# Kernel optimization log

Hardware: AMD Instinct MI355X
Metric: run time of the kernel (lower is better)

## Reference

```python
import jax, jax.numpy as jnp
import numpy as np

D = 43           # d_model for '80k'
H1 = 30          # dense1
H2 = 20          # dense2
FEAT = 8


def _lstm_dir(x, w_ih, w_hh, b_ih, b_hh, reverse):
    # x: [B, T, I]; w_ih: [4H, I]; w_hh: [4H, H]; PyTorch gate order i,f,g,o
    B = x.shape[0]
    H = w_hh.shape[1]
    xs = jnp.swapaxes(x, 0, 1)                 # [T, B, I]
    b = b_ih + b_hh
    xz = xs @ w_ih.T + b                        # precompute input GEMM: [T, B, 4H]

    def step(carry, zt):
        h, c = carry
        z = zt + h @ w_hh.T
        i, f, g, o = jnp.split(z, 4, axis=-1)
        i = jax.nn.sigmoid(i); f = jax.nn.sigmoid(f)
        g = jnp.tanh(g);       o = jax.nn.sigmoid(o)
        c = f * c + i * g
        h = o * jnp.tanh(c)
        return (h, c), h

    h0 = jnp.zeros((B, H), x.dtype)
    _, hs = jax.lax.scan(step, (h0, h0), xz, reverse=reverse)
    return jnp.swapaxes(hs, 0, 1)               # [B, T, H]


def _bilstm(x, wf, wb):
    fwd = _lstm_dir(x, *wf, reverse=False)
    bwd = _lstm_dir(x, *wb, reverse=True)
    return jnp.concatenate([fwd, bwd], axis=-1)  # [B, T, 2H]


def setup_inputs() -> dict:
    key = jax.random.key(0)
    ks = iter(jax.random.split(key, 32))
    s = 0.1
    def rn(shape):
        return (jax.random.normal(next(ks), shape, dtype=jnp.float32) * s)
    inp = {"x": jax.random.normal(next(ks), (256, 2048, FEAT), dtype=jnp.float32)}
    # input projection (LazyLinear -> Linear(FEAT, D))
    inp["w_proj"] = rn((D, FEAT)); inp["b_proj"] = rn((D,))
    # lstm1: input D, hidden D, bidirectional
    for tag, isz in (("1f", D), ("1b", D), ("2f", 2 * D), ("2b", 2 * D)):
        inp[f"w_ih{tag}"] = rn((4 * D, isz))
        inp[f"w_hh{tag}"] = rn((4 * D, D))
        inp[f"b_ih{tag}"] = rn((4 * D,))
        inp[f"b_hh{tag}"] = rn((4 * D,))
    inp["w_d1"] = rn((H1, 2 * D)); inp["b_d1"] = rn((H1,))
    inp["w_d2"] = rn((H2, H1));    inp["b_d2"] = rn((H2,))
    inp["w_out"] = rn((1, H2));    inp["b_out"] = rn((1,))
    return inp


def reference(x, w_proj, b_proj,
              w_ih1f, w_hh1f, b_ih1f, b_hh1f,
              w_ih1b, w_hh1b, b_ih1b, b_hh1b,
              w_ih2f, w_hh2f, b_ih2f, b_hh2f,
              w_ih2b, w_hh2b, b_ih2b, b_hh2b,
              w_d1, b_d1, w_d2, b_d2, w_out, b_out):
    h = x @ w_proj.T + b_proj                                   # [B,T,D]
    h = _bilstm(h, (w_ih1f, w_hh1f, b_ih1f, b_hh1f),
                   (w_ih1b, w_hh1b, b_ih1b, b_hh1b))            # [B,T,2D]
    h = _bilstm(h, (w_ih2f, w_hh2f, b_ih2f, b_hh2f),
                   (w_ih2b, w_hh2b, b_ih2b, b_hh2b))            # [B,T,2D]
    h = jax.nn.relu(h @ w_d1.T + b_d1)
    h = jax.nn.relu(h @ w_d2.T + b_d2)
    return h @ w_out.T + b_out                                  # [B,T,1]
```

## Files before the change

### kernel.cpp

```cpp
#include <hip/hip_runtime.h>
#include <hip/hip_bf16.h>
#include <math.h>

#define DD   43
#define RR   172
#define TT   2048
#define BB   256
#define FEAT 8
#define NH1  30
#define NH2  20

using bf16 = __hip_bfloat16;

__device__ __forceinline__ float ldv(const float* p)  { return *p; }
__device__ __forceinline__ float ldv(const bf16* p)   { return __bfloat162float(*p); }
__device__ __forceinline__ void  stv(float* p, float v) { *p = v; }
__device__ __forceinline__ void  stv(bf16* p,  float v) { *p = __float2bfloat16(v); }

__device__ __forceinline__ float sig_(float x) {
    return 1.0f / (1.0f + __expf(-x));
}
__device__ __forceinline__ float tanh_(float x) {
    float ax = fabsf(x);
    float e  = __expf(-2.0f * ax);
    float t  = (1.0f - e) / (1.0f + e);
    return x < 0.0f ? -t : t;
}

__global__ void prep_kernel(const float* __restrict__ wp, const float* __restrict__ bp,
                            const float* __restrict__ w_ih1f, const float* __restrict__ b_ih1f, const float* __restrict__ b_hh1f,
                            const float* __restrict__ w_ih1b, const float* __restrict__ b_ih1b, const float* __restrict__ b_hh1b,
                            const float* __restrict__ b_ih2f, const float* __restrict__ b_hh2f,
                            const float* __restrict__ b_ih2b, const float* __restrict__ b_hh2b,
                            float* __restrict__ w_eff1, float* __restrict__ b_eff1,
                            float* __restrict__ b_eff2) {
    int tid = blockIdx.x * blockDim.x + threadIdx.x;
    if (tid < 2 * RR) {
        int dir = tid / RR, r = tid % RR;
        const float* w_ih = dir ? w_ih1b : w_ih1f;
        const float* bi   = dir ? b_ih1b : b_ih1f;
        const float* bh   = dir ? b_hh1b : b_hh1f;
        const float* row  = w_ih + (long)r * DD;
        float acc[FEAT];
#pragma unroll
        for (int k = 0; k < FEAT; ++k) acc[k] = 0.0f;
        float bacc = bi[r] + bh[r];
        for (int d = 0; d < DD; ++d) {
            float w = row[d];
            bacc = fmaf(w, bp[d], bacc);
#pragma unroll
            for (int k = 0; k < FEAT; ++k) acc[k] = fmaf(w, wp[d * FEAT + k], acc[k]);
        }
#pragma unroll
        for (int k = 0; k < FEAT; ++k) w_eff1[(long)tid * FEAT + k] = acc[k];
        b_eff1[tid] = bacc;
    } else if (tid < 4 * RR) {
        int j = tid - 2 * RR;
        int dir = j / RR, r = j % RR;
        b_eff2[j] = dir ? (b_ih2b[r] + b_hh2b[r]) : (b_ih2f[r] + b_hh2f[r]);
    }
}

template <int KI, typename TIN, typename TOUT>
__global__ __launch_bounds__(192) void lstm_kernel(
        const TIN* __restrict__ in,
        const float* __restrict__ w_ih_f,
        const float* __restrict__ w_hh_f,
        const float* __restrict__ bias_f,
        const float* __restrict__ w_ih_b,
        const float* __restrict__ w_hh_b,
        const float* __restrict__ bias_b,
        TOUT* __restrict__ out)
{
    const int bid = blockIdx.x;
    const int dir = bid & 1;
    const int b   = bid >> 1;
    const int tid = threadIdx.x;

    const float* w_ih = dir ? w_ih_b : w_ih_f;
    const float* w_hh = dir ? w_hh_b : w_hh_f;
    const float* bias = dir ? bias_b : bias_f;

    __shared__ float xbuf[2][KI];
    __shared__ float hbuf[DD];
    __shared__ float zbuf[RR];

    float wi[KI];
    float wh[DD];
    float bsum = 0.0f, c = 0.0f;
    if (tid < RR) {
        const float* wr = w_ih + (long)tid * KI;
#pragma unroll
        for (int k = 0; k < KI; ++k) wi[k] = wr[k];
        const float* hr = w_hh + (long)tid * DD;
#pragma unroll
        for (int k = 0; k < DD; ++k) wh[k] = hr[k];
        bsum = bias[tid];
    }

    const long t0   = dir ? (TT - 1) : 0;
    const int  step = dir ? -1 : 1;

    if (tid < DD) hbuf[tid] = 0.0f;
    float xnext = 0.0f;
    if (tid < KI) xnext = ldv(&in[((long)b * TT + t0) * KI + tid]);

    TOUT* outp = out + (long)b * TT * (2 * DD) + dir * DD;

    __syncthreads();

    long tcur = t0;
    for (int s = 0; s < TT; ++s) {
        if (tid < KI) xbuf[s & 1][tid] = xnext;
        __syncthreads();

        if (tid < RR) {
            float z = bsum;
            const float* xb = xbuf[s & 1];
#pragma unroll
            for (int k = 0; k < KI; ++k) z = fmaf(wi[k], xb[k], z);
#pragma unroll
            for (int k = 0; k < DD; ++k) z = fmaf(wh[k], hbuf[k], z);
            zbuf[tid] = z;
        }
        long tnext = tcur + step;
        if (s + 1 < TT && tid < KI) xnext = ldv(&in[((long)b * TT + tnext) * KI + tid]);
        __syncthreads();

        if (tid < DD) {
            float zi = zbuf[tid];
            float zf = zbuf[tid + DD];
            float zg = zbuf[tid + 2 * DD];
            float zo = zbuf[tid + 3 * DD];
            float ig = sig_(zi), fg = sig_(zf), gg = tanh_(zg), og = sig_(zo);
            c = fmaf(fg, c, ig * gg);
            float h = og * tanh_(c);
            hbuf[tid] = h;
            stv(&outp[tcur * (2 * DD) + tid], h);
        }
        tcur = tnext;
    }
}

template <typename TIN>
__global__ void head_kernel(const TIN* __restrict__ h2,
                            const float* __restrict__ w1, const float* __restrict__ b1,
                            const float* __restrict__ w2, const float* __restrict__ b2,
                            const float* __restrict__ w3, const float* __restrict__ b3,
                            float* __restrict__ outp) {
    long bt = (long)blockIdx.x * blockDim.x + threadIdx.x;
    if (bt >= (long)BB * TT) return;
    float v[2 * DD];
    const TIN* src = h2 + bt * (2 * DD);
#pragma unroll
    for (int k = 0; k < 2 * DD; ++k) v[k] = ldv(&src[k]);

    float m1[NH1];
#pragma unroll
    for (int j = 0; j < NH1; ++j) {
        float a = b1[j];
        const float* w = w1 + j * (2 * DD);
#pragma unroll
        for (int k = 0; k < 2 * DD; ++k) a = fmaf(w[k], v[k], a);
        m1[j] = fmaxf(a, 0.0f);
    }
    float m2[NH2];
#pragma unroll
    for (int j = 0; j < NH2; ++j) {
        float a = b2[j];
        const float* w = w2 + j * NH1;
#pragma unroll
        for (int k = 0; k < NH1; ++k) a = fmaf(w[k], m1[k], a);
        m2[j] = fmaxf(a, 0.0f);
    }
    float a = b3[0];
#pragma unroll
    for (int k = 0; k < NH2; ++k) a = fmaf(w3[k], m2[k], a);
    outp[bt] = a;
}

extern "C" void kernel_launch(void* const* d_in, const int* in_sizes, int n_in,
                              void* d_out, int out_size, void* d_ws, size_t ws_size,
                              hipStream_t stream) {
    const float* x      = (const float*)d_in[0];
    const float* w_proj = (const float*)d_in[1];
    const float* b_proj = (const float*)d_in[2];
    const float* w_ih1f = (const float*)d_in[3];
    const float* w_hh1f = (const float*)d_in[4];
    const float* b_ih1f = (const float*)d_in[5];
    const float* b_hh1f = (const float*)d_in[6];
    const float* w_ih1b = (const float*)d_in[7];
    const float* w_hh1b = (const float*)d_in[8];
    const float* b_ih1b = (const float*)d_in[9];
    const float* b_hh1b = (const float*)d_in[10];
    const float* w_ih2f = (const float*)d_in[11];
    const float* w_hh2f = (const float*)d_in[12];
    const float* b_ih2f = (const float*)d_in[13];
    const float* b_hh2f = (const float*)d_in[14];
    const float* w_ih2b = (const float*)d_in[15];
    const float* w_hh2b = (const float*)d_in[16];
    const float* b_ih2b = (const float*)d_in[17];
    const float* b_hh2b = (const float*)d_in[18];
    const float* w_d1   = (const float*)d_in[19];
    const float* b_d1   = (const float*)d_in[20];
    const float* w_d2   = (const float*)d_in[21];
    const float* b_d2   = (const float*)d_in[22];
    const float* w_out  = (const float*)d_in[23];
    const float* b_out  = (const float*)d_in[24];
    (void)in_sizes; (void)n_in; (void)out_size;

    float* w_eff1 = (float*)d_ws;
    float* b_eff1 = w_eff1 + 2 * RR * FEAT;
    float* b_eff2 = b_eff1 + 2 * RR;
    char*  big    = (char*)d_ws + 16384;
    size_t avail  = ws_size > 16384 ? ws_size - 16384 : 0;

    const size_t n1 = (size_t)BB * TT * 2 * DD;
    const size_t f1 = n1 * sizeof(float);
    const size_t h1 = n1 * sizeof(bf16);

    int tier;
    if      (avail >= f1 + f1) tier = 0;
    else if (avail >= f1 + h1) tier = 1;
    else                       tier = 2;

    prep_kernel<<<(4 * RR + 191) / 192, 192, 0, stream>>>(
        w_proj, b_proj,
        w_ih1f, b_ih1f, b_hh1f, w_ih1b, b_ih1b, b_hh1b,
        b_ih2f, b_hh2f, b_ih2b, b_hh2b,
        w_eff1, b_eff1, b_eff2);

    const float* weff_f = w_eff1;
    const float* weff_b = w_eff1 + (size_t)RR * FEAT;
    const float* be1_f  = b_eff1;
    const float* be1_b  = b_eff1 + RR;
    const float* be2_f  = b_eff2;
    const float* be2_b  = b_eff2 + RR;
    const int head_blocks = (int)(((long)BB * TT + 255) / 256);

    if (tier == 0) {
        float* out1 = (float*)big;
        float* out2 = (float*)(big + f1);
        lstm_kernel<FEAT, float, float><<<2 * BB, 192, 0, stream>>>(
            x, weff_f, w_hh1f, be1_f, weff_b, w_hh1b, be1_b, out1);
        lstm_kernel<2 * DD, float, float><<<2 * BB, 192, 0, stream>>>(
            out1, w_ih2f, w_hh2f, be2_f, w_ih2b, w_hh2b, be2_b, out2);
        head_kernel<float><<<head_blocks, 256, 0, stream>>>(
            out2, w_d1, b_d1, w_d2, b_d2, w_out, b_out, (float*)d_out);
    } else if (tier == 1) {
        float* out1 = (float*)big;
        bf16*  out2 = (bf16*)(big + f1);
        lstm_kernel<FEAT, float, float><<<2 * BB, 192, 0, stream>>>(
            x, weff_f, w_hh1f, be1_f, weff_b, w_hh1b, be1_b, out1);
        lstm_kernel<2 * DD, float, bf16><<<2 * BB, 192, 0, stream>>>(
            out1, w_ih2f, w_hh2f, be2_f, w_ih2b, w_hh2b, be2_b, out2);
        head_kernel<bf16><<<head_blocks, 256, 0, stream>>>(
            out2, w_d1, b_d1, w_d2, b_d2, w_out, b_out, (float*)d_out);
    } else {
        bf16* out1 = (bf16*)big;
        bf16* out2 = (bf16*)(big + h1);
        lstm_kernel<FEAT, float, bf16><<<2 * BB, 192, 0, stream>>>(
            x, weff_f, w_hh1f, be1_f, weff_b, w_hh1b, be1_b, out1);
        lstm_kernel<2 * DD, bf16, bf16><<<2 * BB, 192, 0, stream>>>(
            out1, w_ih2f, w_hh2f, be2_f, w_ih2b, w_hh2b, be2_b, out2);
        head_kernel<bf16><<<head_blocks, 256, 0, stream>>>(
            out2, w_d1, b_d1, w_d2, b_d2, w_out, b_out, (float*)d_out);
    }
}
```

Measured before the change: 3.973 ms.

## Split LSTM gate dot products across thread pairs with vectorized shared loads

Each gate row's dot product over the concatenated [x, h] vector is now split between two threads, which combine partial sums with a lane shuffle. Blocks grow from 192 to 384 threads. Inputs and hidden state share one double-buffered, float4-aligned shared-memory vector, so reads are vectorized and accumulation uses four independent chains. Gate activations move into the row threads, which leaves only the cell update on the 43 state threads and shortens the serial critical path per timestep. In exchange it adds a shuffle, padding work and more threads per block, which may limit occupancy.

Result: faster. 3.262 ms (-17.9%).

```diff
diff --git a/kernel.cpp b/kernel.cpp
--- a/kernel.cpp
+++ b/kernel.cpp
@@ -62,7 +62,7 @@
 }
 
 template <int KI, typename TIN, typename TOUT>
-__global__ __launch_bounds__(192) void lstm_kernel(
+__global__ __launch_bounds__(384, 3) void lstm_kernel(
         const TIN* __restrict__ in,
         const float* __restrict__ w_ih_f,
         const float* __restrict__ w_hh_f,
@@ -72,6 +72,11 @@
         const float* __restrict__ bias_b,
         TOUT* __restrict__ out)
 {
+    constexpr int K    = KI + DD;
+    constexpr int K4   = (K + 3) / 4;
+    constexpr int H0   = (K4 + 1) / 2;
+    constexpr int KPAD = 8 * H0;
+
     const int bid = blockIdx.x;
     const int dir = bid & 1;
     const int b   = bid >> 1;
@@ -81,64 +86,86 @@
     const float* w_hh = dir ? w_hh_b : w_hh_f;
     const float* bias = dir ? bias_b : bias_f;
 
-    __shared__ float xbuf[2][KI];
-    __shared__ float hbuf[DD];
+    __shared__ __align__(16) float sbuf[2][KPAD];
     __shared__ float zbuf[RR];
 
-    float wi[KI];
-    float wh[DD];
+    const int r  = tid >> 1;
+    const int hf = tid & 1;
+    const int g0 = hf ? H0 : 0;
+    const int gN = hf ? (K4 - H0) : H0;
+
+    float w[4 * H0];
     float bsum = 0.0f, c = 0.0f;
-    if (tid < RR) {
-        const float* wr = w_ih + (long)tid * KI;
-#pragma unroll
-        for (int k = 0; k < KI; ++k) wi[k] = wr[k];
-        const float* hr = w_hh + (long)tid * DD;
-#pragma unroll
-        for (int k = 0; k < DD; ++k) wh[k] = hr[k];
-        bsum = bias[tid];
-    }
-
-    const long t0   = dir ? (TT - 1) : 0;
-    const int  step = dir ? -1 : 1;
-
-    if (tid < DD) hbuf[tid] = 0.0f;
+    if (tid < 2 * RR) {
+#pragma unroll
+        for (int g = 0; g < H0; ++g) {
+#pragma unroll
+            for (int j = 0; j < 4; ++j) {
+                int k = 4 * (g0 + g) + j;
+                float v = 0.0f;
+                if (g < gN && k < K)
+                    v = (k < KI) ? w_ih[(long)r * KI + k]
+                                 : w_hh[(long)r * DD + (k - KI)];
+                w[4 * g + j] = v;
+            }
+        }
+        if (hf == 0) bsum = bias[r];
+    }
+    for (int k = KI + tid; k < KPAD; k += 384) {
+        sbuf[0][k] = 0.0f;
+        sbuf[1][k] = 0.0f;
+    }
+
+    const long t0  = dir ? (TT - 1) : 0;
+    const int  stp = dir ? -1 : 1;
+
     float xnext = 0.0f;
-    if (tid < KI) xnext = ldv(&in[((long)b * TT + t0) * KI + tid]);
+    if (tid < KI) xnext = ldv(in + ((long)b * TT + t0) * KI + tid);
 
     TOUT* outp = out + (long)b * TT * (2 * DD) + dir * DD;
 
     __syncthreads();
 
-    long tcur = t0;
+    long t = t0;
     for (int s = 0; s < TT; ++s) {
-        if (tid < KI) xbuf[s & 1][tid] = xnext;
+        const int cur = s & 1, nxt = cur ^ 1;
+        if (tid < KI) sbuf[cur][tid] = xnext;
         __syncthreads();
 
-        if (tid < RR) {
-            float z = bsum;
-            const float* xb = xbuf[s & 1];
-#pragma unroll
-            for (int k = 0; k < KI; ++k) z = fmaf(wi[k], xb[k], z);
-#pragma unroll
-            for (int k = 0; k < DD; ++k) z = fmaf(wh[k], hbuf[k], z);
-            zbuf[tid] = z;
-        }
-        long tnext = tcur + step;
-        if (s + 1 < TT && tid < KI) xnext = ldv(&in[((long)b * TT + tnext) * KI + tid]);
+        const long tn = t + stp;
+        if (s + 1 < TT && tid < KI) xnext = ldv(in + ((long)b * TT + tn) * KI + tid);
+
+        if (tid < 2 * RR) {
+            const float4* sv = reinterpret_cast<const float4*>(&sbuf[cur][0]) + g0;
+            float a0 = bsum, a1 = 0.0f, a2 = 0.0f, a3 = 0.0f;
+#pragma unroll
+            for (int g = 0; g < H0; ++g) {
+                float4 xv = sv[g];
+                a0 = fmaf(w[4 * g + 0], xv.x, a0);
+                a1 = fmaf(w[4 * g + 1], xv.y, a1);
+                a2 = fmaf(w[4 * g + 2], xv.z, a2);
+                a3 = fmaf(w[4 * g + 3], xv.w, a3);
+            }
+            float z = (a0 + a1) + (a2 + a3);
+            z += __shfl_xor(z, 1);
+            if (hf == 0) {
+                float act = (r >= 2 * DD && r < 3 * DD) ? tanh_(z) : sig_(z);
+                zbuf[r] = act;
+            }
+        }
         __syncthreads();
 
         if (tid < DD) {
-            float zi = zbuf[tid];
-            float zf = zbuf[tid + DD];
-            float zg = zbuf[tid + 2 * DD];
-            float zo = zbuf[tid + 3 * DD];
-            float ig = sig_(zi), fg = sig_(zf), gg = tanh_(zg), og = sig_(zo);
+            float ig = zbuf[tid];
+            float fg = zbuf[tid + DD];
+            float gg = zbuf[tid + 2 * DD];
+            float og = zbuf[tid + 3 * DD];
             c = fmaf(fg, c, ig * gg);
             float h = og * tanh_(c);
-            hbuf[tid] = h;
-            stv(&outp[tcur * (2 * DD) + tid], h);
-        }
-        tcur = tnext;
+            sbuf[nxt][KI + tid] = h;
+            stv(&outp[t * (2 * DD) + tid], h);
+        }
+        t = tn;
     }
 }
 
@@ -241,27 +268,27 @@
     if (tier == 0) {
         float* out1 = (float*)big;
         float* out2 = (float*)(big + f1);
-        lstm_kernel<FEAT, float, float><<<2 * BB, 192, 0, stream>>>(
+        lstm_kernel<FEAT, float, float><<<2 * BB, 384, 0, stream>>>(
             x, weff_f, w_hh1f, be1_f, weff_b, w_hh1b, be1_b, out1);
-        lstm_kernel<2 * DD, float, float><<<2 * BB, 192, 0, stream>>>(
+        lstm_kernel<2 * DD, float, float><<<2 * BB, 384, 0, stream>>>(
             out1, w_ih2f, w_hh2f, be2_f, w_ih2b, w_hh2b, be2_b, out2);
         head_kernel<float><<<head_blocks, 256, 0, stream>>>(
             out2, w_d1, b_d1, w_d2, b_d2, w_out, b_out, (float*)d_out);
     } else if (tier == 1) {
         float* out1 = (float*)big;
         bf16*  out2 = (bf16*)(big + f1);
-        lstm_kernel<FEAT, float, float><<<2 * BB, 192, 0, stream>>>(
+        lstm_kernel<FEAT, float, float><<<2 * BB, 384, 0, stream>>>(
             x, weff_f, w_hh1f, be1_f, weff_b, w_hh1b, be1_b, out1);
-        lstm_kernel<2 * DD, float, bf16><<<2 * BB, 192, 0, stream>>>(
+        lstm_kernel<2 * DD, float, bf16><<<2 * BB, 384, 0, stream>>>(
             out1, w_ih2f, w_hh2f, be2_f, w_ih2b, w_hh2b, be2_b, out2);
         head_kernel<bf16><<<head_blocks, 256, 0, stream>>>(
             out2, w_d1, b_d1, w_d2, b_d2, w_out, b_out, (float*)d_out);
     } else {
         bf16* out1 = (bf16*)big;
         bf16* out2 = (bf16*)(big + h1);
-        lstm_kernel<FEAT, float, bf16><<<2 * BB, 192, 0, stream>>>(
+        lstm_kernel<FEAT, float, bf16><<<2 * BB, 384, 0, stream>>>(
             x, weff_f, w_hh1f, be1_f, weff_b, w_hh1b, be1_b, out1);
-        lstm_kernel<2 * DD, bf16, bf16><<<2 * BB, 192, 0, stream>>>(
+        lstm_kernel<2 * DD, bf16, bf16><<<2 * BB, 384, 0, stream>>>(
             out1, w_ih2f, w_hh2f, be2_f, w_ih2b, w_hh2b, be2_b, out2);
         head_kernel<bf16><<<head_blocks, 256, 0, stream>>>(
             out2, w_d1, b_d1, w_d2, b_d2, w_out, b_out, (float*)d_out);
```

## Batch LSTM recurrence over 16 sequences per block using bf16 MFMA

Applied to the files above, without the earlier changes.

Replaces the per-sequence scalar FMA LSTM kernel with a block that handles 16 batch rows at once. At each timestep the input and recurrent projections run as bf16 16x16x32 MFMA ops against concatenated, padded weight fragments held in registers. A prep kernel builds the padded bf16 weight layouts, and both intermediate activations are now stored as bf16, dropping the fp32 tier logic. The intent is to raise arithmetic throughput and cut the sequential per-step cost. The trade-offs are reduced precision (bf16 weights, inputs and hidden state) and far fewer blocks, 32 instead of 512, leaving most CUs idle.

Measured after the change: 5.277 ms. +32.8%, slower.

```diff
diff --git a/kernel.cpp b/kernel.cpp
--- a/kernel.cpp
+++ b/kernel.cpp
@@ -4,22 +4,28 @@
 
 #define DD   43
 #define RR   172
+#define NPAD 176
 #define TT   2048
 #define BB   256
 #define FEAT 8
+#define MB   16
 #define NH1  30
 #define NH2  20
 
 using bf16 = __hip_bfloat16;
+typedef __attribute__((ext_vector_type(8))) short bf16x8;
+typedef __attribute__((ext_vector_type(4))) float f32x4;
 
 __device__ __forceinline__ float ldv(const float* p)  { return *p; }
 __device__ __forceinline__ float ldv(const bf16* p)   { return __bfloat162float(*p); }
 __device__ __forceinline__ void  stv(float* p, float v) { *p = v; }
 __device__ __forceinline__ void  stv(bf16* p,  float v) { *p = __float2bfloat16(v); }
 
-__device__ __forceinline__ float sig_(float x) {
-    return 1.0f / (1.0f + __expf(-x));
-}
+__device__ __forceinline__ short f2b(float f) {
+    bf16 h = __float2bfloat16(f);
+    return *reinterpret_cast<short*>(&h);
+}
+__device__ __forceinline__ float sig_(float x) { return 1.0f / (1.0f + __expf(-x)); }
 __device__ __forceinline__ float tanh_(float x) {
     float ax = fabsf(x);
     float e  = __expf(-2.0f * ax);
@@ -27,118 +33,229 @@
     return x < 0.0f ? -t : t;
 }
 
-__global__ void prep_kernel(const float* __restrict__ wp, const float* __restrict__ bp,
-                            const float* __restrict__ w_ih1f, const float* __restrict__ b_ih1f, const float* __restrict__ b_hh1f,
-                            const float* __restrict__ w_ih1b, const float* __restrict__ b_ih1b, const float* __restrict__ b_hh1b,
-                            const float* __restrict__ b_ih2f, const float* __restrict__ b_hh2f,
-                            const float* __restrict__ b_ih2b, const float* __restrict__ b_hh2b,
-                            float* __restrict__ w_eff1, float* __restrict__ b_eff1,
-                            float* __restrict__ b_eff2) {
-    int tid = blockIdx.x * blockDim.x + threadIdx.x;
-    if (tid < 2 * RR) {
-        int dir = tid / RR, r = tid % RR;
-        const float* w_ih = dir ? w_ih1b : w_ih1f;
-        const float* bi   = dir ? b_ih1b : b_ih1f;
-        const float* bh   = dir ? b_hh1b : b_hh1f;
-        const float* row  = w_ih + (long)r * DD;
-        float acc[FEAT];
-#pragma unroll
-        for (int k = 0; k < FEAT; ++k) acc[k] = 0.0f;
-        float bacc = bi[r] + bh[r];
-        for (int d = 0; d < DD; ++d) {
-            float w = row[d];
-            bacc = fmaf(w, bp[d], bacc);
-#pragma unroll
-            for (int k = 0; k < FEAT; ++k) acc[k] = fmaf(w, wp[d * FEAT + k], acc[k]);
-        }
-#pragma unroll
-        for (int k = 0; k < FEAT; ++k) w_eff1[(long)tid * FEAT + k] = acc[k];
-        b_eff1[tid] = bacc;
-    } else if (tid < 4 * RR) {
-        int j = tid - 2 * RR;
-        int dir = j / RR, r = j % RR;
-        b_eff2[j] = dir ? (b_ih2b[r] + b_hh2b[r]) : (b_ih2f[r] + b_hh2f[r]);
-    }
-}
-
-template <int KI, typename TIN, typename TOUT>
-__global__ __launch_bounds__(192) void lstm_kernel(
-        const TIN* __restrict__ in,
-        const float* __restrict__ w_ih_f,
-        const float* __restrict__ w_hh_f,
-        const float* __restrict__ bias_f,
-        const float* __restrict__ w_ih_b,
-        const float* __restrict__ w_hh_b,
-        const float* __restrict__ bias_b,
-        TOUT* __restrict__ out)
+__global__ void prep_kernel(
+    const float* __restrict__ wp, const float* __restrict__ bp,
+    const float* __restrict__ w_ih1f, const float* __restrict__ w_hh1f,
+    const float* __restrict__ b_ih1f, const float* __restrict__ b_hh1f,
+    const float* __restrict__ w_ih1b, const float* __restrict__ w_hh1b,
+    const float* __restrict__ b_ih1b, const float* __restrict__ b_hh1b,
+    const float* __restrict__ w_ih2f, const float* __restrict__ w_hh2f,
+    const float* __restrict__ b_ih2f, const float* __restrict__ b_hh2f,
+    const float* __restrict__ w_ih2b, const float* __restrict__ w_hh2b,
+    const float* __restrict__ b_ih2b, const float* __restrict__ b_hh2b,
+    short* __restrict__ W1, short* __restrict__ W2,
+    float* __restrict__ bias1, float* __restrict__ bias2)
 {
-    const int bid = blockIdx.x;
-    const int dir = bid & 1;
-    const int b   = bid >> 1;
-    const int tid = threadIdx.x;
-
-    const float* w_ih = dir ? w_ih_b : w_ih_f;
-    const float* w_hh = dir ? w_hh_b : w_hh_f;
-    const float* bias = dir ? bias_b : bias_f;
-
-    __shared__ float xbuf[2][KI];
-    __shared__ float hbuf[DD];
-    __shared__ float zbuf[RR];
-
-    float wi[KI];
-    float wh[DD];
-    float bsum = 0.0f, c = 0.0f;
-    if (tid < RR) {
-        const float* wr = w_ih + (long)tid * KI;
-#pragma unroll
-        for (int k = 0; k < KI; ++k) wi[k] = wr[k];
-        const float* hr = w_hh + (long)tid * DD;
-#pragma unroll
-        for (int k = 0; k < DD; ++k) wh[k] = hr[k];
-        bsum = bias[tid];
-    }
-
-    const long t0   = dir ? (TT - 1) : 0;
-    const int  step = dir ? -1 : 1;
-
-    if (tid < DD) hbuf[tid] = 0.0f;
-    float xnext = 0.0f;
-    if (tid < KI) xnext = ldv(&in[((long)b * TT + t0) * KI + tid]);
-
-    TOUT* outp = out + (long)b * TT * (2 * DD) + dir * DD;
-
+    const int S1 = 2 * NPAD * 96, S2 = 2 * NPAD * 160, S3 = 2 * NPAD;
+    int idx = blockIdx.x * blockDim.x + threadIdx.x;
+    if (idx < S1) {
+        int dir = idx / (NPAD * 96), rem = idx % (NPAD * 96);
+        int n = rem / 96, k = rem % 96;
+        const float* wih = dir ? w_ih1b : w_ih1f;
+        const float* whh = dir ? w_hh1b : w_hh1f;
+        float v = 0.0f;
+        if (n < RR) {
+            if (k < FEAT) {
+                for (int d = 0; d < DD; ++d) v = fmaf(wih[n * DD + d], wp[d * FEAT + k], v);
+            } else if (k >= 32 && k < 32 + DD) {
+                v = whh[n * DD + (k - 32)];
+            }
+        }
+        W1[idx] = f2b(v);
+    } else if (idx < S1 + S2) {
+        int j = idx - S1;
+        int dir = j / (NPAD * 160), rem = j % (NPAD * 160);
+        int n = rem / 160, k = rem % 160;
+        const float* wih = dir ? w_ih2b : w_ih2f;
+        const float* whh = dir ? w_hh2b : w_hh2f;
+        float v = 0.0f;
+        if (n < RR) {
+            if (k < 2 * DD)                 v = wih[n * (2 * DD) + k];
+            else if (k >= 96 && k < 96 + DD) v = whh[n * DD + (k - 96)];
+        }
+        W2[j] = f2b(v);
+    } else if (idx < S1 + S2 + S3) {
+        int j = idx - S1 - S2;
+        int dir = j / NPAD, n = j % NPAD;
+        float v = 0.0f;
+        if (n < RR) {
+            const float* wih = dir ? w_ih1b : w_ih1f;
+            const float* bi  = dir ? b_ih1b : b_ih1f;
+            const float* bh  = dir ? b_hh1b : b_hh1f;
+            v = bi[n] + bh[n];
+            for (int d = 0; d < DD; ++d) v = fmaf(wih[n * DD + d], bp[d], v);
+        }
+        bias1[j] = v;
+    } else if (idx < S1 + S2 + 2 * S3) {
+        int j = idx - S1 - S2 - S3;
+        int dir = j / NPAD, n = j % NPAD;
+        float v = 0.0f;
+        if (n < RR) {
+            const float* bi = dir ? b_ih2b : b_ih2f;
+            const float* bh = dir ? b_hh2b : b_hh2f;
+            v = bi[n] + bh[n];
+        }
+        bias2[j] = v;
+    }
+}
+
+template <int KSX, bool XRAW>
+__global__ __launch_bounds__(512, 2) void lstm_mfma(
+    const void*  __restrict__ in_,
+    const short* __restrict__ Wb,
+    const float* __restrict__ bias,
+    bf16* __restrict__ out)
+{
+    constexpr int KS   = KSX + 2;
+    constexpr int KPAD = KS * 32;
+
+    const int dir   = blockIdx.x & 1;
+    const int btile = blockIdx.x >> 1;
+    const int tid   = threadIdx.x;
+    const int lane  = tid & 63;
+    const int wv    = tid >> 6;
+    const int ln15  = lane & 15;
+    const int lg    = lane >> 4;
+
+    __shared__ __align__(16) short hbuf[MB][72];
+    __shared__ float zact[MB][177];
+
+    const int nt = (wv < 3) ? 2 : 1;
+
+    bf16x8 wfrag[2][KS];
+    float  bv[2];
+    bool   isg[2];
+    {
+        const short* Wd = Wb + (size_t)dir * NPAD * KPAD;
+#pragma unroll
+        for (int ti = 0; ti < 2; ++ti) {
+            int tile = ti ? (8 + wv) : wv;
+            int n = tile * 16 + ln15;
+            isg[ti] = (n >= 2 * DD && n < 3 * DD);
+            if (ti < nt) {
+#pragma unroll
+                for (int ks = 0; ks < KS; ++ks)
+                    wfrag[ti][ks] = *reinterpret_cast<const bf16x8*>(
+                        Wd + (size_t)n * KPAD + ks * 32 + lg * 8);
+                bv[ti] = bias[dir * NPAD + n];
+            } else {
+#pragma unroll
+                for (int ks = 0; ks < KS; ++ks) wfrag[ti][ks] = bf16x8(0);
+                bv[ti] = 0.0f;
+            }
+        }
+    }
+
+    const int p0 = tid;
+    const int b0 = p0 / DD, d0 = p0 % DD;
+    const int p1 = tid + 512;
+    const bool has1 = (p1 < MB * DD);
+    const int b1 = has1 ? p1 / DD : 0, d1 = has1 ? p1 % DD : 0;
+    float c0 = 0.0f, c1 = 0.0f;
+
+    for (int i = tid; i < MB * 72; i += 512) ((short*)hbuf)[i] = 0;
+
+    const long t00   = dir ? (TT - 1) : 0;
+    const int  stp   = dir ? -1 : 1;
+    const long bbase = (long)(btile * MB + ln15);
+
+    union U { unsigned u[4]; bf16x8 v; };
+    U xc[KSX], xn[KSX];
+
+    auto load_x = [&](long t, U (&xf)[KSX]) {
+        if constexpr (XRAW) {
+            if (lg == 0) {
+                const float* xp = (const float*)in_ + (bbase * TT + t) * FEAT;
+                float4 v0 = *reinterpret_cast<const float4*>(xp);
+                float4 v1 = *reinterpret_cast<const float4*>(xp + 4);
+                xf[0].u[0] = ((unsigned)(unsigned short)f2b(v0.y) << 16) | (unsigned short)f2b(v0.x);
+                xf[0].u[1] = ((unsigned)(unsigned short)f2b(v0.w) << 16) | (unsigned short)f2b(v0.z);
+                xf[0].u[2] = ((unsigned)(unsigned short)f2b(v1.y) << 16) | (unsigned short)f2b(v1.x);
+                xf[0].u[3] = ((unsigned)(unsigned short)f2b(v1.w) << 16) | (unsigned short)f2b(v1.z);
+            } else {
+#pragma unroll
+                for (int j = 0; j < 4; ++j) xf[0].u[j] = 0u;
+            }
+        } else {
+            const short* xp = (const short*)in_ + (bbase * TT + t) * (2 * DD);
+#pragma unroll
+            for (int ks = 0; ks < KSX; ++ks) {
+                int k0 = ks * 32 + lg * 8;
+#pragma unroll
+                for (int j = 0; j < 4; ++j) {
+                    int k = k0 + 2 * j;
+                    xf[ks].u[j] = (k < 2 * DD) ? *reinterpret_cast<const unsigned*>(xp + k) : 0u;
+                }
+            }
+        }
+    };
+
+    load_x(t00, xc);
     __syncthreads();
 
-    long tcur = t0;
+    long t = t00;
     for (int s = 0; s < TT; ++s) {
-        if (tid < KI) xbuf[s & 1][tid] = xnext;
+        bf16x8 ah0 = *reinterpret_cast<const bf16x8*>(&hbuf[ln15][lg * 8]);
+        bf16x8 ah1 = *reinterpret_cast<const bf16x8*>(&hbuf[ln15][32 + lg * 8]);
+        if (s + 1 < TT) load_x(t + stp, xn);
+
+        f32x4 acc0 = {bv[0], bv[0], bv[0], bv[0]};
+#pragma unroll
+        for (int ks = 0; ks < KSX; ++ks)
+            acc0 = __builtin_amdgcn_mfma_f32_16x16x32_bf16(xc[ks].v, wfrag[0][ks], acc0, 0, 0, 0);
+        acc0 = __builtin_amdgcn_mfma_f32_16x16x32_bf16(ah0, wfrag[0][KSX],     acc0, 0, 0, 0);
+        acc0 = __builtin_amdgcn_mfma_f32_16x16x32_bf16(ah1, wfrag[0][KSX + 1], acc0, 0, 0, 0);
+
+        f32x4 acc1 = {bv[1], bv[1], bv[1], bv[1]};
+        if (nt == 2) {
+#pragma unroll
+            for (int ks = 0; ks < KSX; ++ks)
+                acc1 = __builtin_amdgcn_mfma_f32_16x16x32_bf16(xc[ks].v, wfrag[1][ks], acc1, 0, 0, 0);
+            acc1 = __builtin_amdgcn_mfma_f32_16x16x32_bf16(ah0, wfrag[1][KSX],     acc1, 0, 0, 0);
+            acc1 = __builtin_amdgcn_mfma_f32_16x16x32_bf16(ah1, wfrag[1][KSX + 1], acc1, 0, 0, 0);
+        }
+
+        {
+            int n0 = wv * 16 + ln15;
+#pragma unroll
+            for (int r = 0; r < 4; ++r) {
+                float v = acc0[r];
+                zact[lg * 4 + r][n0] = isg[0] ? tanh_(v) : sig_(v);
+            }
+            if (nt == 2) {
+                int n1 = (8 + wv) * 16 + ln15;
+#pragma unroll
+                for (int r = 0; r < 4; ++r) {
+                    float v = acc1[r];
+                    zact[lg * 4 + r][n1] = isg[1] ? tanh_(v) : sig_(v);
+                }
+            }
+        }
         __syncthreads();
 
-        if (tid < RR) {
-            float z = bsum;
-            const float* xb = xbuf[s & 1];
-#pragma unroll
-            for (int k = 0; k < KI; ++k) z = fmaf(wi[k], xb[k], z);
-#pragma unroll
-            for (int k = 0; k < DD; ++k) z = fmaf(wh[k], hbuf[k], z);
-            zbuf[tid] = z;
-        }
-        long tnext = tcur + step;
-        if (s + 1 < TT && tid < KI) xnext = ldv(&in[((long)b * TT + tnext) * KI + tid]);
+        {
+            float ig = zact[b0][d0], fg = zact[b0][d0 + DD];
+            float gg = zact[b0][d0 + 2 * DD], og = zact[b0][d0 + 3 * DD];
+            c0 = fmaf(fg, c0, ig * gg);
+            float h = og * tanh_(c0);
+            hbuf[b0][d0] = f2b(h);
+            out[((long)(btile * MB + b0) * TT + t) * (2 * DD) + dir * DD + d0] = __float2bfloat16(h);
+            if (has1) {
+                float ig1 = zact[b1][d1], fg1 = zact[b1][d1 + DD];
+                float gg1 = zact[b1][d1 + 2 * DD], og1 = zact[b1][d1 + 3 * DD];
+                c1 = fmaf(fg1, c1, ig1 * gg1);
+                float h1 = og1 * tanh_(c1);
+                hbuf[b1][d1] = f2b(h1);
+                out[((long)(btile * MB + b1) * TT + t) * (2 * DD) + dir * DD + d1] = __float2bfloat16(h1);
+            }
+        }
         __syncthreads();
 
-        if (tid < DD) {
-            float zi = zbuf[tid];
-            float zf = zbuf[tid + DD];
-            float zg = zbuf[tid + 2 * DD];
-            float zo = zbuf[tid + 3 * DD];
-            float ig = sig_(zi), fg = sig_(zf), gg = tanh_(zg), og = sig_(zo);
-            c = fmaf(fg, c, ig * gg);
-            float h = og * tanh_(c);
-            hbuf[tid] = h;
-            stv(&outp[tcur * (2 * DD) + tid], h);
-        }
-        tcur = tnext;
+#pragma unroll
+        for (int ks = 0; ks < KSX; ++ks)
+#pragma unroll
+            for (int j = 0; j < 4; ++j) xc[ks].u[j] = xn[ks].u[j];
+        t += stp;
     }
 }
 
@@ -207,63 +324,28 @@
     const float* b_d2   = (const float*)d_in[22];
     const float* w_out  = (const float*)d_in[23];
     const float* b_out  = (const float*)d_in[24];
-    (void)in_sizes; (void)n_in; (void)out_size;
-
-    float* w_eff1 = (float*)d_ws;
-    float* b_eff1 = w_eff1 + 2 * RR * FEAT;
-    float* b_eff2 = b_eff1 + 2 * RR;
-    char*  big    = (char*)d_ws + 16384;
-    size_t avail  = ws_size > 16384 ? ws_size - 16384 : 0;
-
-    const size_t n1 = (size_t)BB * TT * 2 * DD;
-    const size_t f1 = n1 * sizeof(float);
-    const size_t h1 = n1 * sizeof(bf16);
-
-    int tier;
-    if      (avail >= f1 + f1) tier = 0;
-    else if (avail >= f1 + h1) tier = 1;
-    else                       tier = 2;
-
-    prep_kernel<<<(4 * RR + 191) / 192, 192, 0, stream>>>(
-        w_proj, b_proj,
-        w_ih1f, b_ih1f, b_hh1f, w_ih1b, b_ih1b, b_hh1b,
-        b_ih2f, b_hh2f, b_ih2b, b_hh2b,
-        w_eff1, b_eff1, b_eff2);
-
-    const float* weff_f = w_eff1;
-    const float* weff_b = w_eff1 + (size_t)RR * FEAT;
-    const float* be1_f  = b_eff1;
-    const float* be1_b  = b_eff1 + RR;
-    const float* be2_f  = b_eff2;
-    const float* be2_b  = b_eff2 + RR;
-    const int head_blocks = (int)(((long)BB * TT + 255) / 256);
-
-    if (tier == 0) {
-        float* out1 = (float*)big;
-        float* out2 = (float*)(big + f1);
-        lstm_kernel<FEAT, float, float><<<2 * BB, 192, 0, stream>>>(
-            x, weff_f, w_hh1f, be1_f, weff_b, w_hh1b, be1_b, out1);
-        lstm_kernel<2 * DD, float, float><<<2 * BB, 192, 0, stream>>>(
-            out1, w_ih2f, w_hh2f, be2_f, w_ih2b, w_hh2b, be2_b, out2);
-        head_kernel<float><<<head_blocks, 256, 0, stream>>>(
-            out2, w_d1, b_d1, w_d2, b_d2, w_out, b_out, (float*)d_out);
-    } else if (tier == 1) {
-        float* out1 = (float*)big;
-        bf16*  out2 = (bf16*)(big + f1);
-        lstm_kernel<FEAT, float, float><<<2 * BB, 192, 0, stream>>>(
-            x, weff_f, w_hh1f, be1_f, weff_b, w_hh1b, be1_b, out1);
-        lstm_kernel<2 * DD, float, bf16><<<2 * BB, 192, 0, stream>>>(
-            out1, w_ih2f, w_hh2f, be2_f, w_ih2b, w_hh2b, be2_b, out2);
-        head_kernel<bf16><<<head_blocks, 256, 0, stream>>>(
-            out2, w_d1, b_d1, w_d2, b_d2, w_out, b_out, (float*)d_out);
-    } else {
-        bf16* out1 = (bf16*)big;
-        bf16* out2 = (bf16*)(big + h1);
-        lstm_kernel<FEAT, float, bf16><<<2 * BB, 192, 0, stream>>>(
-            x, weff_f, w_hh1f, be1_f, weff_b, w_hh1b, be1_b, out1);
-        lstm_kernel<2 * DD, bf16, bf16><<<2 * BB, 192, 0, stream>>>(
-            out1, w_ih2f, w_hh2f, be2_f, w_ih2b, w_hh2b, be2_b, out2);
-        head_kernel<bf16><<<head_blocks, 256, 0, stream>>>(
-            out2, w_d1, b_d1, w_d2, b_d2, w_out, b_out, (float*)d_out);
-    }
-}
+    (void)in_sizes; (void)n_in; (void)out_size; (void)ws_size;
+
+    char* wsb = (char*)d_ws;
+    short* W1    = (short*)(wsb);
+    short* W2    = (short*)(wsb + 135168);
+    float* bias1 = (float*)(wsb + 135168 + 112640);
+    float* bias2 = (float*)(wsb + 135168 + 112640 + 1408);
+    const size_t o_big = 262144;
+    const size_t n1    = (size_t)BB * TT * 2 * DD;
+    bf16* out1 = (bf16*)(wsb + o_big);
+    bf16* out2 = (bf16*)(wsb + o_big + n1 * sizeof(bf16));
+
+    {
+        const int total = 2 * NPAD * 96 + 2 * NPAD * 160 + 2 * (2 * NPAD);
+        prep_kernel<<<(total + 255) / 256, 256, 0, stream>>>(
+            w_proj, b_proj,
+            w_ih1f, w_hh1f, b_ih1f, b_hh1f, w_ih1b, w_hh1b, b_ih1b, b_hh1b,
+            w_ih2f, w_hh2f, b_ih2f, b_hh2f, w_ih2b, w_hh2b, b_ih2b, b_hh2b,
+            W1, W2, bias1, bias2);
+    }
+    lstm_mfma<1, true><<<2 * (BB / MB), 512, 0, stream>>>(x, W1, bias1, out1);
+    lstm_mfma<3, false><<<2 * (BB / MB), 512, 0, stream>>>(out1, W2, bias2, out2);
+    head_kernel<bf16><<<(int)(((long)BB * TT + 255) / 256), 256, 0, stream>>>(
+        out2, w_d1, b_d1, w_d2, b_d2, w_out, b_out, (float*)d_out);
+}
```
